# Kernel tuning notes

Hardware: AMD Instinct MI355X
Metric: run time of the kernel (lower is better)

Reference implementation:

```python
import jax, jax.numpy as jnp
import numpy as np

B, T, N, D, H, MH = 8, 13, 128, 4, 64, 128


def setup_inputs() -> dict:
    key = jax.random.key(0)
    ks = iter(jax.random.split(key, 32))
    def w(shape):
        return (jax.random.normal(next(ks), shape, jnp.float32) / np.sqrt(shape[0])).astype(jnp.float32)
    def b(n):
        return jnp.zeros((n,), jnp.float32)
    return {
        "A": jax.random.normal(next(ks), (B, N, N), jnp.float32),
        "X": jax.random.normal(next(ks), (B, T, N, D), jnp.float32),
        "Wm1": w((2 * H, MH)), "bm1": b(MH),
        "Wm2": w((MH, H)), "bm2": b(H),
        "Wir": w((D, H)), "bir": b(H),
        "Wii": w((D, H)), "bii": b(H),
        "Win": w((D, H)), "bin_": b(H),
        "Whr": w((H, H)), "Whi": w((H, H)), "Whh": w((H, H)),
        "Wmr": w((H, H)), "Wmi": w((H, H)), "Wmn": w((H, H)),
        "Wo1": w((H, H)), "bo1": b(H),
        "Wo2": w((H, H)), "bo2": b(H),
        "Wo3": w((H, D)), "bo3": b(D),
        "log_sigma": jnp.log(jnp.float32(0.1)),
    }


def _project_adjacency(A, temp=1.0, eps=1e-6):
    A = 0.5 * (A + jnp.swapaxes(A, -1, -2))
    A = jax.nn.sigmoid(A / temp)
    n = A.shape[-1]
    A = A * (1.0 - jnp.eye(n, dtype=A.dtype))
    return A / (A.sum(axis=-1, keepdims=True) + eps)


def reference(A, X, Wm1, bm1, Wm2, bm2, Wir, bir, Wii, bii, Win, bin_,
              Whr, Whi, Whh, Wmr, Wmi, Wmn, Wo1, bo1, Wo2, bo2, Wo3, bo3, log_sigma):
    Ap = _project_adjacency(A)
    Bb, Tt, Nn, Dd = X.shape
    Hh = Whr.shape[0]
    sigma = jnp.clip(jnp.exp(log_sigma), 1e-4, 10.0)
    count = Bb * Nn * Dd
    const = 0.5 * count * jnp.log(2.0 * jnp.pi * sigma * sigma)
    inv2s2 = 1.0 / (2.0 * sigma * sigma)

    def step(carry, xt_tgt):
        hidden, ll = carry
        x_t, tgt = xt_tgt
        # all-pairs message: pre[b,i,j] = [h_i, h_j]
        pre = jnp.concatenate([
            jnp.broadcast_to(hidden[:, :, None, :], (Bb, Nn, Nn, Hh)),
            jnp.broadcast_to(hidden[:, None, :, :], (Bb, Nn, Nn, Hh)),
        ], axis=-1)
        msg = jnp.tanh(jnp.tanh(pre @ Wm1 + bm1) @ Wm2 + bm2)
        # agg[b,j] = sum_i A[b,i,j] * msg[b,i,j]
        agg = jnp.einsum('bij,bijh->bjh', Ap, msg)
        r = jax.nn.sigmoid(x_t @ Wir + bir + hidden @ Whr + agg @ Wmr)
        i = jax.nn.sigmoid(x_t @ Wii + bii + hidden @ Whi + agg @ Wmi)
        n = jnp.tanh(x_t @ Win + bin_ + r * (hidden @ Whh) + agg @ Wmn)
        h_new = (1.0 - i) * n + i * hidden
        pred = jax.nn.relu(h_new @ Wo1 + bo1)
        pred = jax.nn.relu(pred @ Wo2 + bo2)
        pred = x_t + pred @ Wo3 + bo3
        nll = const + jnp.sum((tgt - pred) ** 2) * inv2s2
        return (h_new, ll - nll), pred

    hidden0 = jnp.zeros((Bb, Nn, Hh), X.dtype)
    xs = (jnp.moveaxis(X[:, :-1], 1, 0), jnp.moveaxis(X[:, 1:], 1, 0))  # time-major
    (_, loglik), preds = jax.lax.scan(step, (hidden0, jnp.float32(0.0)), xs)
    X_pred = jnp.moveaxis(preds, 0, 1)  # [B, T-1, N, D]
    return (X_pred, loglik)
```

## Files before the change

### kernel.cpp

```cpp
#include <hip/hip_runtime.h>
#include <math.h>

#define B_ 8
#define N_ 128
#define H_ 64
#define MH_ 128
#define D_ 4
#define TSTEPS 12
#define NBLK 256

typedef __attribute__((ext_vector_type(8))) short bf16x8;
typedef __attribute__((ext_vector_type(4))) float f32x4;
typedef __attribute__((ext_vector_type(4))) unsigned u32x4;
typedef unsigned uint32;

__device__ __forceinline__ float fast_tanh(float x) {
    float t = __builtin_amdgcn_exp2f(x * 2.8853900817779268f);
    return 1.0f - 2.0f * __builtin_amdgcn_rcpf(t + 1.0f);
}
__device__ __forceinline__ float fast_sigmoid(float x) {
    float t = __builtin_amdgcn_exp2f(x * -1.4426950408889634f);
    return __builtin_amdgcn_rcpf(1.0f + t);
}
__device__ __forceinline__ unsigned short f2bf(float x) {
    unsigned u = __builtin_bit_cast(unsigned, x);
    u += 0x7fffu + ((u >> 16) & 1u);
    return (unsigned short)(u >> 16);
}
__device__ __forceinline__ uint32 cvtpk(float lo, float hi) {
    uint32 r;
    asm("v_cvt_pk_bf16_f32 %0, %1, %2" : "=v"(r) : "v"(lo), "v"(hi));
    return r;
}

constexpr int PB_STRIDE = 65536;
constexpr int CTRLu = 11 * PB_STRIDE;
constexpr int CTRL_BYTES = (32 * 16 + 2) * 4;

__global__ __launch_bounds__(1024, 4) void fused(
    const float* __restrict__ A, const float* __restrict__ X,
    const float* __restrict__ Wm1, const float* __restrict__ bm1,
    const float* __restrict__ Wm2, const float* __restrict__ bm2,
    const float* __restrict__ Wir, const float* __restrict__ bir,
    const float* __restrict__ Wii, const float* __restrict__ bii,
    const float* __restrict__ Win, const float* __restrict__ bin_,
    const float* __restrict__ Whr, const float* __restrict__ Whi, const float* __restrict__ Whh,
    const float* __restrict__ Wmr, const float* __restrict__ Wmi, const float* __restrict__ Wmn,
    const float* __restrict__ Wo1, const float* __restrict__ bo1,
    const float* __restrict__ Wo2, const float* __restrict__ bo2,
    const float* __restrict__ Wo3, const float* __restrict__ bo3,
    const float* __restrict__ lsg,
    uint32* wsU, float* __restrict__ out)
{
    __shared__ __align__(16) unsigned short wm2f[8192];
    __shared__ __align__(16) float WamL[12288];
    __shared__ __align__(16) float Wm1L[16384];
    __shared__ float Qj[4][128], apRow[4][128], rs[128], bmS[128];
    __shared__ float aggbuf[4][4][64];
    __shared__ float sAgg[4][64], sAm[4][192], sHP[4][192];
    __shared__ float sHist[TSTEPS][4][64];
    __shared__ float sX[4][4];

    const int bid = blockIdx.x, tid = threadIdx.x;
    const int b = bid >> 5;
    const int j0 = (bid & 31) << 2;
    const int wave = tid >> 6, lane = tid & 63;
    const int jj = wave >> 2;
    const int wvj = wave & 3;
    const int l15 = lane & 15, g = lane >> 4;
    const int myI0 = wvj * 32;

    int*   cntBase = (int*)(wsU + CTRLu);
    int*   cntW    = cntBase + (b * 4 + wvj) * 16;
    int*   cntPub  = cntBase + (b * 4 + (j0 >> 5)) * 16;
    float* sseG    = (float*)(wsU + CTRLu + 512);
    int*   doneG   = (int*)(wsU + CTRLu + 513);
    const float* Ab = A + b * 16384;

    {
        int i = tid & 127, q = tid >> 7;
        float part = 0.f;
        int jlo = q * 16;
        #pragma unroll 4
        for (int j2 = jlo; j2 < jlo + 16; ++j2)
            if (j2 != i)
                part += fast_sigmoid(0.5f * (Ab[i * 128 + j2] + Ab[j2 * 128 + i]));
        ((float*)aggbuf)[q * 128 + i] = part;
    }
    __syncthreads();
    if (tid < 128) {
        const float* f = (const float*)aggbuf;
        float s = 0.f;
        #pragma unroll
        for (int c = 0; c < 8; ++c) s += f[c * 128 + tid];
        rs[tid] = s + 1e-6f;
        bmS[tid] = bm1[tid];
    }
    __syncthreads();
    if (tid < 512) {
        int i = tid & 127, h = tid >> 7, jc = j0 + h;
        float s = (i == jc) ? 0.f
                : fast_sigmoid(0.5f * (Ab[i * 128 + jc] + Ab[jc * 128 + i]));
        apRow[h][i] = s / rs[i];
    }
    for (int idx = tid; idx < 8192; idx += 1024) {
        int kt = idx >> 11, nt = (idx >> 9) & 3, ln = (idx >> 3) & 63, e = idx & 7;
        int k = kt * 32 + (ln >> 4) * 8 + e, n = nt * 16 + (ln & 15);
        wm2f[idx] = f2bf(Wm2[k * 64 + n]);
    }
    for (int idx = tid; idx < 12288; idx += 1024) {
        int k = idx / 192, c = idx % 192;
        WamL[idx] = ((c < 64) ? Wmr : (c < 128) ? Wmi : Wmn)[k * 64 + (c & 63)];
    }
    for (int idx = tid; idx < 16384; idx += 1024)
        Wm1L[idx] = Wm1[idx];
    if (tid < 512) Qj[tid >> 7][tid & 127] = 0.f;
    if (tid < 768) sHP[tid / 192][tid % 192] = 0.f;
    if (tid < 256) sAgg[tid >> 6][tid & 63] = 0.f;
    __syncthreads();

    for (int t = 0; t < TSTEPS; ++t) {
        const uint32* Psrc = wsU + (t - 1) * PB_STRIDE + b * 8192;
        if (t > 0) {
            const int target = 32 * t;
            int guard = 0;
            while (__hip_atomic_load(cntW, __ATOMIC_RELAXED, __HIP_MEMORY_SCOPE_AGENT) < target
                   && guard < (1 << 20)) {
                __builtin_amdgcn_s_sleep(1);
                ++guard;
            }
            __builtin_amdgcn_fence(__ATOMIC_ACQUIRE, "workgroup");
        }

        f32x4 acc[2][4];
        #pragma unroll
        for (int mt = 0; mt < 2; ++mt)
            #pragma unroll
            for (int nt = 0; nt < 4; ++nt) {
                f32x4 z = {0.f, 0.f, 0.f, 0.f};
                acc[mt][nt] = z;
            }
        #pragma unroll
        for (int kt = 0; kt < 4; ++kt) {
            int k0 = kt * 32 + g * 8;
            bf16x8 bf[4];
            #pragma unroll
            for (int nt = 0; nt < 4; ++nt)
                bf[nt] = *(const bf16x8*)&wm2f[((kt * 4 + nt) * 64 + lane) << 3];
            f32x4 qa = *(const f32x4*)&Qj[jj][k0];
            f32x4 qb = *(const f32x4*)&Qj[jj][k0 + 4];
            bf16x8 af[2];
            #pragma unroll
            for (int mt = 0; mt < 2; ++mt) {
                int row = myI0 + mt * 16 + l15;
                float pe[8];
                if (t > 0) {
                    u32x4 pv = *(const u32x4*)(Psrc + row * 64 + kt * 16 + g * 4);
                    #pragma unroll
                    for (int c = 0; c < 4; ++c) {
                        pe[2 * c]     = __builtin_bit_cast(float, pv[c] << 16);
                        pe[2 * c + 1] = __builtin_bit_cast(float, pv[c] & 0xFFFF0000u);
                    }
                } else {
                    #pragma unroll
                    for (int e = 0; e < 8; ++e) pe[e] = bmS[k0 + e];
                }
                float tv[8];
                #pragma unroll
                for (int e = 0; e < 4; ++e) {
                    tv[e]     = fast_tanh(pe[e] + qa[e]);
                    tv[4 + e] = fast_tanh(pe[4 + e] + qb[e]);
                }
                u32x4 aw;
                aw[0] = cvtpk(tv[0], tv[1]); aw[1] = cvtpk(tv[2], tv[3]);
                aw[2] = cvtpk(tv[4], tv[5]); aw[3] = cvtpk(tv[6], tv[7]);
                af[mt] = __builtin_bit_cast(bf16x8, aw);
            }
            #pragma unroll
            for (int mt = 0; mt < 2; ++mt)
                #pragma unroll
                for (int nt = 0; nt < 4; ++nt)
                    acc[mt][nt] = __builtin_amdgcn_mfma_f32_16x16x32_bf16(af[mt], bf[nt], acc[mt][nt], 0, 0, 0);
        }
        {
            float bmv[4];
            #pragma unroll
            for (int nt = 0; nt < 4; ++nt) bmv[nt] = bm2[nt * 16 + l15];
            float pagg[4] = {0.f, 0.f, 0.f, 0.f};
            #pragma unroll
            for (int mt = 0; mt < 2; ++mt) {
                float w[4];
                #pragma unroll
                for (int v = 0; v < 4; ++v) w[v] = apRow[jj][myI0 + mt * 16 + g * 4 + v];
                #pragma unroll
                for (int nt = 0; nt < 4; ++nt)
                    #pragma unroll
                    for (int v = 0; v < 4; ++v)
                        pagg[nt] += w[v] * fast_tanh(acc[mt][nt][v] + bmv[nt]);
            }
            #pragma unroll
            for (int nt = 0; nt < 4; ++nt) {
                pagg[nt] += __shfl_xor(pagg[nt], 16);
                pagg[nt] += __shfl_xor(pagg[nt], 32);
            }
            if (lane < 16)
                #pragma unroll
                for (int nt = 0; nt < 4; ++nt)
                    atomicAdd(&sAgg[jj][nt * 16 + lane], pagg[nt]);
        }
        __syncthreads();

        if (tid < 384) {
            int pr = tid / 192, c = tid % 192;
            int r0 = pr * 2, r1 = r0 + 1;
            float a0 = 0.f, a1 = 0.f;
            #pragma unroll 8
            for (int k = 0; k < 64; ++k) {
                float w = WamL[k * 192 + c];
                a0 += sAgg[r0][k] * w; a1 += sAgg[r1][k] * w;
            }
            sAm[r0][c] = a0; sAm[r1][c] = a1;
        } else if (tid >= 960 && tid < 976) {
            int q = tid - 960;
            int r = q >> 2, d = q & 3, jrow = j0 + r;
            sX[r][d] = X[((b * 13 + t) * 128 + jrow) * 4 + d];
        }
        __syncthreads();
        if (tid < 256) {
            int r = tid >> 6, o = tid & 63;
            float xr = bir[o], xi = bii[o], xn = bin_[o];
            #pragma unroll
            for (int d = 0; d < 4; ++d) {
                float xv = sX[r][d];
                xr += xv * Wir[d * 64 + o];
                xi += xv * Wii[d * 64 + o];
                xn += xv * Win[d * 64 + o];
            }
            float hprev = (t > 0) ? sHist[t - 1][r][o] : 0.f;
            float rr = fast_sigmoid(xr + sHP[r][o]       + sAm[r][o]);
            float ig = fast_sigmoid(xi + sHP[r][64 + o]  + sAm[r][64 + o]);
            float nn = fast_tanh  (xn + rr * sHP[r][128 + o] + sAm[r][128 + o]);
            sHist[t][r][o] = (1.0f - ig) * nn + ig * hprev;
        }
        __syncthreads();

        if (t < TSTEPS - 1) {
            if (tid < 128 || (tid >= 512 && tid < 640)) {
                int hi2 = (tid >= 512) ? 1 : 0;
                int o = tid - hi2 * 512;
                int r0 = hi2 * 2, r1 = r0 + 1;
                float a0 = bmS[o], a1 = bmS[o];
                #pragma unroll 8
                for (int k = 0; k < 64; ++k) {
                    float w = Wm1L[k * 128 + o];
                    a0 += sHist[t][r0][k] * w; a1 += sHist[t][r1][k] * w;
                }
                uint32 u0 = cvtpk(a0, __shfl_down(a0, 1));
                uint32 u1 = cvtpk(a1, __shfl_down(a1, 1));
                if ((o & 1) == 0) {
                    uint32* base = wsU + t * PB_STRIDE + b * 8192;
                    __hip_atomic_store(base + (j0 + r0) * 64 + (o >> 1), u0,
                                       __ATOMIC_RELAXED, __HIP_MEMORY_SCOPE_AGENT);
                    __hip_atomic_store(base + (j0 + r1) * 64 + (o >> 1), u1,
                                       __ATOMIC_RELAXED, __HIP_MEMORY_SCOPE_AGENT);
                }
                asm volatile("s_waitcnt vmcnt(0)" ::: "memory");
                if (lane == 0)
                    __hip_atomic_fetch_add(cntPub, 1, __ATOMIC_RELAXED, __HIP_MEMORY_SCOPE_AGENT);
            } else if (tid < 256 || (tid >= 640 && tid < 768)) {
                int hi2 = (tid >= 640) ? 1 : 0;
                int oo = tid - 128 - hi2 * 512;
                int r0 = hi2 * 2, r1 = r0 + 1;
                float a0 = 0.f, a1 = 0.f;
                #pragma unroll 8
                for (int k = 0; k < 64; ++k) {
                    float w = Wm1L[(64 + k) * 128 + oo];
                    a0 += sHist[t][r0][k] * w; a1 += sHist[t][r1][k] * w;
                }
                Qj[r0][oo] = a0; Qj[r1][oo] = a1;
            } else if (tid < 448 || (tid >= 768 && tid < 960)) {
                int hi2 = (tid >= 768) ? 1 : 0;
                int c = tid - 256 - hi2 * 512;
                int r0 = hi2 * 2, r1 = r0 + 1;
                const float* W = (c < 64) ? Whr : (c < 128) ? Whi : Whh;
                int oc = c & 63;
                float a0 = 0.f, a1 = 0.f;
                #pragma unroll 8
                for (int k = 0; k < 64; ++k) {
                    float w = W[k * 64 + oc];
                    a0 += sHist[t][r0][k] * w; a1 += sHist[t][r1][k] * w;
                }
                sHP[r0][c] = a0; sHP[r1][c] = a1;
            } else if (tid >= 448 && tid < 512) {
                int o = tid - 448;
                #pragma unroll
                for (int r = 0; r < 4; ++r) sAgg[r][o] = 0.f;
            }
        }
        __syncthreads();
    }

    float ssePart = 0.f;
    {
        float* scratch = &((float*)aggbuf)[wave * 64];
        #pragma unroll
        for (int inst = 0; inst < 3; ++inst) {
            int idx = wave + (inst << 4);
            int tt = idx >> 2, r = idx & 3;
            float a = bo1[lane];
            #pragma unroll 8
            for (int k = 0; k < 64; ++k) a += sHist[tt][r][k] * Wo1[k * 64 + lane];
            scratch[lane] = fmaxf(a, 0.f);
            asm volatile("s_waitcnt lgkmcnt(0)" ::: "memory");
            __builtin_amdgcn_sched_barrier(0);
            float a2 = bo2[lane];
            #pragma unroll 8
            for (int k = 0; k < 64; ++k) a2 += scratch[k] * Wo2[k * 64 + lane];
            scratch[lane] = fmaxf(a2, 0.f);
            asm volatile("s_waitcnt lgkmcnt(0)" ::: "memory");
            __builtin_amdgcn_sched_barrier(0);
            if (lane < 16) {
                int d = lane >> 2, q = lane & 3;
                float a3 = 0.f;
                #pragma unroll 4
                for (int k = q * 16; k < q * 16 + 16; ++k) a3 += scratch[k] * Wo3[k * 4 + d];
                a3 += __shfl_xor(a3, 1);
                a3 += __shfl_xor(a3, 2);
                if (q == 0) {
                    int jrow = j0 + r;
                    float xv = X[((b * 13 + tt) * 128 + jrow) * 4 + d];
                    float tg = X[((b * 13 + tt + 1) * 128 + jrow) * 4 + d];
                    float p = xv + a3 + bo3[d];
                    out[((b * TSTEPS + tt) * 128 + jrow) * 4 + d] = p;
                    float df = tg - p;
                    ssePart += df * df;
                }
            }
            asm volatile("s_waitcnt lgkmcnt(0)" ::: "memory");
            __builtin_amdgcn_sched_barrier(0);
        }
    }
    #pragma unroll
    for (int d = 1; d < 64; d <<= 1) ssePart += __shfl_xor(ssePart, d);
    if (lane == 0) rs[wave] = ssePart;
    __syncthreads();

    if (tid == 0) {
        float s = 0.f;
        #pragma unroll
        for (int w = 0; w < 16; ++w) s += rs[w];
        atomicAdd(sseG, s);
        int prev = __hip_atomic_fetch_add(doneG, 1, __ATOMIC_ACQ_REL, __HIP_MEMORY_SCOPE_AGENT);
        if (prev == NBLK - 1) {
            float sse = __hip_atomic_load(sseG, __ATOMIC_RELAXED, __HIP_MEMORY_SCOPE_AGENT);
            float ls = lsg[0];
            float sigma = fminf(fmaxf(expf(ls), 1e-4f), 10.0f);
            float c = 0.5f * 4096.0f * logf(2.0f * 3.14159265358979323846f * sigma * sigma);
            float inv2s2 = 1.0f / (2.0f * sigma * sigma);
            out[B_ * TSTEPS * N_ * D_] = -(12.0f * c + sse * inv2s2);
        }
    }
}

extern "C" void kernel_launch(void* const* d_in, const int* in_sizes, int n_in,
                              void* d_out, int out_size, void* d_ws, size_t ws_size,
                              hipStream_t stream)
{
    const float* A    = (const float*)d_in[0];
    const float* X    = (const float*)d_in[1];
    const float* Wm1  = (const float*)d_in[2];
    const float* bm1  = (const float*)d_in[3];
    const float* Wm2  = (const float*)d_in[4];
    const float* bm2  = (const float*)d_in[5];
    const float* Wir  = (const float*)d_in[6];
    const float* bir  = (const float*)d_in[7];
    const float* Wii  = (const float*)d_in[8];
    const float* bii  = (const float*)d_in[9];
    const float* Win  = (const float*)d_in[10];
    const float* bin_ = (const float*)d_in[11];
    const float* Whr  = (const float*)d_in[12];
    const float* Whi  = (const float*)d_in[13];
    const float* Whh  = (const float*)d_in[14];
    const float* Wmr  = (const float*)d_in[15];
    const float* Wmi  = (const float*)d_in[16];
    const float* Wmn  = (const float*)d_in[17];
    const float* Wo1  = (const float*)d_in[18];
    const float* bo1  = (const float*)d_in[19];
    const float* Wo2  = (const float*)d_in[20];
    const float* bo2  = (const float*)d_in[21];
    const float* Wo3  = (const float*)d_in[22];
    const float* bo3  = (const float*)d_in[23];
    const float* lsg  = (const float*)d_in[24];
    uint32* wsU = (uint32*)d_ws;
    float* out = (float*)d_out;

    hipMemsetAsync((char*)d_ws + (size_t)CTRLu * 4, 0, CTRL_BYTES, stream);

    hipLaunchKernelGGL(fused, dim3(NBLK), dim3(1024), 0, stream,
                       A, X, Wm1, bm1, Wm2, bm2, Wir, bir, Wii, bii, Win, bin_,
                       Whr, Whi, Whh, Wmr, Wmi, Wmn, Wo1, bo1, Wo2, bo2, Wo3, bo3,
                       lsg, wsU, out);
}
```

Baseline: 201.2 us.

## Fuse GRU update with next-step projections via redundant per-wave gates and shuffles

Every wave now recomputes the GRU gate update for its two rows and passes the new hidden state between lanes with shuffles. Each wave then feeds it straight into its slice of the Wm1, Qj and hidden-projection matvecs, which removes one block-wide barrier per timestep. The hidden-projection buffer is double-buffered so the next step's values can be written while the current ones are still being read. The agg@Wam matvec is also split across all 768 threads with a k-split and a shuffle reduction, instead of using 384 threads. In exchange, the gate math is repeated redundantly across 8 waves, and serial lane shuffles replace shared-memory reads.

```diff
diff --git a/kernel.cpp b/kernel.cpp
--- a/kernel.cpp
+++ b/kernel.cpp
@@ -57,7 +57,8 @@
     __shared__ __align__(16) float Wm1L[16384];
     __shared__ float Qj[4][128], apRow[4][128], rs[128], bmS[128];
     __shared__ float aggbuf[4][4][64];
-    __shared__ float sAgg[4][64], sAm[4][192], sHP[4][192];
+    __shared__ float sAgg[4][64], sAm[4][192];
+    __shared__ float sHPbuf[2][4][192];
     __shared__ float sHist[TSTEPS][4][64];
     __shared__ float sX[4][4];
 
@@ -69,6 +70,9 @@
     const int wvj = wave & 3;
     const int l15 = lane & 15, g = lane >> 4;
     const int myI0 = wvj * 32;
+    const int pr = wave >> 3;
+    const int wloc = wave & 7;
+    const int r0 = pr * 2, r1 = r0 + 1;
 
     int*   cntBase = (int*)(wsU + CTRLu);
     int*   cntW    = cntBase + (b * 4 + wvj) * 16;
@@ -115,12 +119,13 @@
     for (int idx = tid; idx < 16384; idx += 1024)
         Wm1L[idx] = Wm1[idx];
     if (tid < 512) Qj[tid >> 7][tid & 127] = 0.f;
-    if (tid < 768) sHP[tid / 192][tid % 192] = 0.f;
+    if (tid < 768) sHPbuf[0][tid / 192][tid % 192] = 0.f;
     if (tid < 256) sAgg[tid >> 6][tid & 63] = 0.f;
     __syncthreads();
 
     for (int t = 0; t < TSTEPS; ++t) {
         const uint32* Psrc = wsU + (t - 1) * PB_STRIDE + b * 8192;
+        const int cur = t & 1, nxt = cur ^ 1;
         if (t > 0) {
             const int target = 32 * t;
             int guard = 0;
@@ -210,91 +215,115 @@
         }
         __syncthreads();
 
-        if (tid < 384) {
-            int pr = tid / 192, c = tid % 192;
-            int r0 = pr * 2, r1 = r0 + 1;
+        if (tid < 768) {
+            int og = (wave << 5) + (lane & 31);
+            int apr = og / 192, c = og % 192;
+            int ar0 = apr * 2, ar1 = ar0 + 1;
+            int klo = (lane >> 5) << 5;
             float a0 = 0.f, a1 = 0.f;
             #pragma unroll 8
-            for (int k = 0; k < 64; ++k) {
+            for (int k = klo; k < klo + 32; ++k) {
                 float w = WamL[k * 192 + c];
-                a0 += sAgg[r0][k] * w; a1 += sAgg[r1][k] * w;
-            }
-            sAm[r0][c] = a0; sAm[r1][c] = a1;
-        } else if (tid >= 960 && tid < 976) {
-            int q = tid - 960;
+                a0 += sAgg[ar0][k] * w; a1 += sAgg[ar1][k] * w;
+            }
+            a0 += __shfl_xor(a0, 32);
+            a1 += __shfl_xor(a1, 32);
+            if (lane < 32) { sAm[ar0][c] = a0; sAm[ar1][c] = a1; }
+        } else if (tid >= 768 && tid < 784) {
+            int q = tid - 768;
             int r = q >> 2, d = q & 3, jrow = j0 + r;
             sX[r][d] = X[((b * 13 + t) * 128 + jrow) * 4 + d];
         }
         __syncthreads();
-        if (tid < 256) {
-            int r = tid >> 6, o = tid & 63;
-            float xr = bir[o], xi = bii[o], xn = bin_[o];
+
+        {
+            int o = lane;
+            float w1[4], w2[4], w3[4];
             #pragma unroll
             for (int d = 0; d < 4; ++d) {
-                float xv = sX[r][d];
-                xr += xv * Wir[d * 64 + o];
-                xi += xv * Wii[d * 64 + o];
-                xn += xv * Win[d * 64 + o];
-            }
-            float hprev = (t > 0) ? sHist[t - 1][r][o] : 0.f;
-            float rr = fast_sigmoid(xr + sHP[r][o]       + sAm[r][o]);
-            float ig = fast_sigmoid(xi + sHP[r][64 + o]  + sAm[r][64 + o]);
-            float nn = fast_tanh  (xn + rr * sHP[r][128 + o] + sAm[r][128 + o]);
-            sHist[t][r][o] = (1.0f - ig) * nn + ig * hprev;
-        }
-        __syncthreads();
-
-        if (t < TSTEPS - 1) {
-            if (tid < 128 || (tid >= 512 && tid < 640)) {
-                int hi2 = (tid >= 512) ? 1 : 0;
-                int o = tid - hi2 * 512;
-                int r0 = hi2 * 2, r1 = r0 + 1;
-                float a0 = bmS[o], a1 = bmS[o];
-                #pragma unroll 8
-                for (int k = 0; k < 64; ++k) {
-                    float w = Wm1L[k * 128 + o];
-                    a0 += sHist[t][r0][k] * w; a1 += sHist[t][r1][k] * w;
-                }
-                uint32 u0 = cvtpk(a0, __shfl_down(a0, 1));
-                uint32 u1 = cvtpk(a1, __shfl_down(a1, 1));
-                if ((o & 1) == 0) {
-                    uint32* base = wsU + t * PB_STRIDE + b * 8192;
-                    __hip_atomic_store(base + (j0 + r0) * 64 + (o >> 1), u0,
-                                       __ATOMIC_RELAXED, __HIP_MEMORY_SCOPE_AGENT);
-                    __hip_atomic_store(base + (j0 + r1) * 64 + (o >> 1), u1,
-                                       __ATOMIC_RELAXED, __HIP_MEMORY_SCOPE_AGENT);
-                }
-                asm volatile("s_waitcnt vmcnt(0)" ::: "memory");
-                if (lane == 0)
-                    __hip_atomic_fetch_add(cntPub, 1, __ATOMIC_RELAXED, __HIP_MEMORY_SCOPE_AGENT);
-            } else if (tid < 256 || (tid >= 640 && tid < 768)) {
-                int hi2 = (tid >= 640) ? 1 : 0;
-                int oo = tid - 128 - hi2 * 512;
-                int r0 = hi2 * 2, r1 = r0 + 1;
-                float a0 = 0.f, a1 = 0.f;
-                #pragma unroll 8
-                for (int k = 0; k < 64; ++k) {
-                    float w = Wm1L[(64 + k) * 128 + oo];
-                    a0 += sHist[t][r0][k] * w; a1 += sHist[t][r1][k] * w;
-                }
-                Qj[r0][oo] = a0; Qj[r1][oo] = a1;
-            } else if (tid < 448 || (tid >= 768 && tid < 960)) {
-                int hi2 = (tid >= 768) ? 1 : 0;
-                int c = tid - 256 - hi2 * 512;
-                int r0 = hi2 * 2, r1 = r0 + 1;
-                const float* W = (c < 64) ? Whr : (c < 128) ? Whi : Whh;
-                int oc = c & 63;
-                float a0 = 0.f, a1 = 0.f;
-                #pragma unroll 8
-                for (int k = 0; k < 64; ++k) {
-                    float w = W[k * 64 + oc];
-                    a0 += sHist[t][r0][k] * w; a1 += sHist[t][r1][k] * w;
-                }
-                sHP[r0][c] = a0; sHP[r1][c] = a1;
-            } else if (tid >= 448 && tid < 512) {
-                int o = tid - 448;
-                #pragma unroll
-                for (int r = 0; r < 4; ++r) sAgg[r][o] = 0.f;
+                w1[d] = Wir[d * 64 + o]; w2[d] = Wii[d * 64 + o]; w3[d] = Win[d * 64 + o];
+            }
+            float hr0, hr1;
+            {
+                float xr = bir[o], xi = bii[o], xn = bin_[o];
+                #pragma unroll
+                for (int d = 0; d < 4; ++d) {
+                    float xv = sX[r0][d];
+                    xr += xv * w1[d]; xi += xv * w2[d]; xn += xv * w3[d];
+                }
+                float hprev = (t > 0) ? sHist[t - 1][r0][o] : 0.f;
+                float rr = fast_sigmoid(xr + sHPbuf[cur][r0][o]       + sAm[r0][o]);
+                float ig = fast_sigmoid(xi + sHPbuf[cur][r0][64 + o]  + sAm[r0][64 + o]);
+                float nn = fast_tanh  (xn + rr * sHPbuf[cur][r0][128 + o] + sAm[r0][128 + o]);
+                hr0 = (1.0f - ig) * nn + ig * hprev;
+            }
+            {
+                float xr = bir[o], xi = bii[o], xn = bin_[o];
+                #pragma unroll
+                for (int d = 0; d < 4; ++d) {
+                    float xv = sX[r1][d];
+                    xr += xv * w1[d]; xi += xv * w2[d]; xn += xv * w3[d];
+                }
+                float hprev = (t > 0) ? sHist[t - 1][r1][o] : 0.f;
+                float rr = fast_sigmoid(xr + sHPbuf[cur][r1][o]       + sAm[r1][o]);
+                float ig = fast_sigmoid(xi + sHPbuf[cur][r1][64 + o]  + sAm[r1][64 + o]);
+                float nn = fast_tanh  (xn + rr * sHPbuf[cur][r1][128 + o] + sAm[r1][128 + o]);
+                hr1 = (1.0f - ig) * nn + ig * hprev;
+            }
+
+            const bool isLast = (t == TSTEPS - 1);
+            if (wloc == 7) {
+                sHist[t][r0][o] = hr0;
+                sHist[t][r1][o] = hr1;
+                if (pr == 0) {
+                    #pragma unroll
+                    for (int r = 0; r < 4; ++r) sAgg[r][o] = 0.f;
+                }
+            } else if (!isLast) {
+                if (wloc < 2) {
+                    int oo = (wloc << 6) + lane;
+                    float a0 = bmS[oo], a1 = bmS[oo];
+                    #pragma unroll 8
+                    for (int k = 0; k < 64; ++k) {
+                        float w = Wm1L[k * 128 + oo];
+                        a0 += __shfl(hr0, k) * w;
+                        a1 += __shfl(hr1, k) * w;
+                    }
+                    uint32 u0 = cvtpk(a0, __shfl_down(a0, 1));
+                    uint32 u1 = cvtpk(a1, __shfl_down(a1, 1));
+                    if ((oo & 1) == 0) {
+                        uint32* base = wsU + t * PB_STRIDE + b * 8192;
+                        __hip_atomic_store(base + (j0 + r0) * 64 + (oo >> 1), u0,
+                                           __ATOMIC_RELAXED, __HIP_MEMORY_SCOPE_AGENT);
+                        __hip_atomic_store(base + (j0 + r1) * 64 + (oo >> 1), u1,
+                                           __ATOMIC_RELAXED, __HIP_MEMORY_SCOPE_AGENT);
+                    }
+                    asm volatile("s_waitcnt vmcnt(0)" ::: "memory");
+                    if (lane == 0)
+                        __hip_atomic_fetch_add(cntPub, 1, __ATOMIC_RELAXED, __HIP_MEMORY_SCOPE_AGENT);
+                } else if (wloc < 4) {
+                    int oo = ((wloc - 2) << 6) + lane;
+                    float a0 = 0.f, a1 = 0.f;
+                    #pragma unroll 8
+                    for (int k = 0; k < 64; ++k) {
+                        float w = Wm1L[(64 + k) * 128 + oo];
+                        a0 += __shfl(hr0, k) * w;
+                        a1 += __shfl(hr1, k) * w;
+                    }
+                    Qj[r0][oo] = a0; Qj[r1][oo] = a1;
+                } else {
+                    const float* W = (wloc == 4) ? Whr : (wloc == 5) ? Whi : Whh;
+                    int c = ((wloc - 4) << 6) + lane;
+                    int oc = lane;
+                    float a0 = 0.f, a1 = 0.f;
+                    #pragma unroll 8
+                    for (int k = 0; k < 64; ++k) {
+                        float w = W[k * 64 + oc];
+                        a0 += __shfl(hr0, k) * w;
+                        a1 += __shfl(hr1, k) * w;
+                    }
+                    sHPbuf[nxt][r0][c] = a0; sHPbuf[nxt][r1][c] = a1;
+                }
             }
         }
         __syncthreads();
```

New measurement: 231.1 us. +14.9%, slower.
